# Optimization experiments

Hardware: AMD Instinct MI355X
Metric: run time of the kernel (lower is better)

The kernel has to match this reference:

```python
import jax, jax.numpy as jnp
import numpy as np

SLOPE = 25.0   # fast_sigmoid surrogate slope (affects backward only)
THRESH = 1.0   # snntorch Leaky default threshold

@jax.custom_vjp
def spike(x):
    # Heaviside forward, fast-sigmoid surrogate backward
    return (x > 0).astype(x.dtype)

def _spike_fwd(x):
    return spike(x), x

def _spike_bwd(x, g):
    return (g / (SLOPE * jnp.abs(x) + 1.0) ** 2,)

spike.defvjp(_spike_fwd, _spike_bwd)


def setup_inputs() -> dict:
    key = jax.random.key(0)
    ks = jax.random.split(key, 16)
    B, T, F = 512, 1024, 64
    SNN, H, HOR = 128, 128, 24
    s = 0.05
    inp = {
        "x": jax.random.normal(ks[0], (B, T, F), jnp.float32),
        "proj_w": jax.random.normal(ks[1], (SNN, F), jnp.float32) * s,
        "proj_b": jnp.zeros((SNN,), jnp.float32),
        "beta1": jnp.full((SNN,), 0.9, jnp.float32),
        "beta2": jnp.full((SNN,), 0.9, jnp.float32),
        "gru_w_ih": jax.random.normal(ks[2], (3 * H, F + SNN), jnp.float32) * s,
        "gru_w_hh": jax.random.normal(ks[3], (3 * H, H), jnp.float32) * s,
        "gru_b_ih": jnp.zeros((3 * H,), jnp.float32),
        "gru_b_hh": jnp.zeros((3 * H,), jnp.float32),
        "attn_w1": jax.random.normal(ks[4], (H // 2, H), jnp.float32) * s,
        "attn_b1": jnp.zeros((H // 2,), jnp.float32),
        "attn_w2": jax.random.normal(ks[5], (1, H // 2), jnp.float32) * s,
        "attn_b2": jnp.zeros((1,), jnp.float32),
        "head_w": jax.random.normal(ks[6], (HOR, H), jnp.float32) * s,
        "head_b": jnp.zeros((HOR,), jnp.float32),
    }
    return inp


def reference(x, proj_w, proj_b, beta1, beta2,
              gru_w_ih, gru_w_hh, gru_b_ih, gru_b_hh,
              attn_w1, attn_b1, attn_w2, attn_b2, head_w, head_b):
    b1 = jnp.clip(beta1, 0.0, 0.99)
    b2 = jnp.clip(beta2, 0.0, 0.99)

    delta = x[:, 1:, :] - x[:, :-1, :]   # (B, T-1, F)
    raw = x[:, 1:, :]
    h_s = delta @ proj_w.T + proj_b      # (B, T-1, SNN)

    B = x.shape[0]
    SNN = proj_w.shape[0]

    # snntorch Leaky (subtract reset, reset from previous step's spike):
    # mem_t = beta*mem_{t-1} + in_t - spk_{t-1}*thr ; spk_t = H(mem_t - thr)
    def snn_step(carry, inp_t):
        m1, s1, m2, s2 = carry
        m1 = b1 * m1 + inp_t - s1 * THRESH
        s1n = spike(m1 - THRESH)
        m2 = b2 * m2 + s1n - s2 * THRESH
        s2n = spike(m2 - THRESH)
        return (m1, s1n, m2, s2n), m2

    z = jnp.zeros((B, SNN), x.dtype)
    _, mem_rec = jax.lax.scan(snn_step, (z, z, z, z), jnp.swapaxes(h_s, 0, 1))
    h_snn = jnp.swapaxes(mem_rec, 0, 1)             # (B, T-1, SNN)

    h_comb = jnp.concatenate([raw, h_snn], axis=-1)  # (B, T-1, F+SNN)

    # GRU (PyTorch gate layout: r, z, n)
    H = gru_w_hh.shape[1]
    x_proj = h_comb @ gru_w_ih.T + gru_b_ih          # (B, T-1, 3H)

    def gru_step(h, xp):
        gh = h @ gru_w_hh.T + gru_b_hh
        xr, xz, xn = jnp.split(xp, 3, axis=-1)
        hr, hz, hn = jnp.split(gh, 3, axis=-1)
        r = jax.nn.sigmoid(xr + hr)
        zg = jax.nn.sigmoid(xz + hz)
        n = jnp.tanh(xn + r * hn)
        h_new = (1.0 - zg) * n + zg * h
        return h_new, h_new

    h0 = jnp.zeros((B, H), x.dtype)
    _, gru_seq = jax.lax.scan(gru_step, h0, jnp.swapaxes(x_proj, 0, 1))
    gru_out = jnp.swapaxes(gru_seq, 0, 1)            # (B, T-1, H)

    # Temporal attention over time (dim=1)
    scores = jax.nn.relu(gru_out @ attn_w1.T + attn_b1) @ attn_w2.T + attn_b2  # (B, T-1, 1)
    w = jax.nn.softmax(scores, axis=1)
    h_ann = (w * gru_out).sum(axis=1)                # (B, H)

    return h_ann @ head_w.T + head_b                 # (B, horizon)
```

## Files before the change

kernel.cpp:

```cpp
#include <hip/hip_runtime.h>

typedef unsigned short u16;
typedef __attribute__((ext_vector_type(8))) short short8;
typedef __attribute__((ext_vector_type(4))) float f32x4;

__device__ __forceinline__ u16 f2bf(float f) {
  union { float f; unsigned u; } v; v.f = f;
  unsigned r = v.u + 0x7fffu + ((v.u >> 16) & 1u);
  return (u16)(r >> 16);
}
__device__ __forceinline__ u16 truncbf(float f) {
  union { float f; unsigned u; } v; v.f = f;
  return (u16)(v.u >> 16);
}
__device__ __forceinline__ float bf2f(u16 h) {
  union { unsigned u; float f; } v; v.u = ((unsigned)h) << 16;
  return v.f;
}
__device__ __forceinline__ void gll16(const void* g, void* l) {
  __builtin_amdgcn_global_load_lds((const __attribute__((address_space(1))) unsigned*)g,
                                   (__attribute__((address_space(3))) unsigned*)l, 16, 0, 0);
}
__device__ __forceinline__ void bar_lds() {
  asm volatile("s_waitcnt lgkmcnt(0)" ::: "memory");
  __builtin_amdgcn_s_barrier();
  asm volatile("" ::: "memory");
}

#define BATCH 512
#define TS 1023
#define NF 64
#define NS 128
#define NH 128
#define NG 384
#define NC 192
#define TCH 341

__global__ void k_prep(const float* __restrict__ wih, const float* __restrict__ w1,
                       u16* __restrict__ wihb, u16* __restrict__ w1b) {
  int i = blockIdx.x * 256 + threadIdx.x;
  if (i < NG * NC) wihb[i] = f2bf(wih[i]);
  if (i < 64 * NH) w1b[i] = f2bf(w1[i]);
}

__global__ __launch_bounds__(256, 2) void k_front(const float* __restrict__ x,
                                                  const float* __restrict__ pw,
                                                  const float* __restrict__ pb,
                                                  const float* __restrict__ beta1,
                                                  const float* __restrict__ beta2,
                                                  u16* __restrict__ hcomb) {
  __shared__ float hst[64 * 138];
  const int tid = threadIdx.x, lane = tid & 63, w = tid >> 6;
  const int m16 = lane & 15, quad = lane >> 4;
  const int b = blockIdx.x;
  const float* xb = x + (long)b * 65536;

  const int tm = (w >> 1) * 32, nn = (w & 1) * 64;

  short8 bh[2][4], bl[2][4];
  #pragma unroll
  for (int kc = 0; kc < 2; ++kc)
    #pragma unroll
    for (int ni = 0; ni < 4; ++ni) {
      const float* src = pw + (nn + ni * 16 + m16) * 64 + kc * 32 + quad * 8;
      f32x4 v0 = *(const f32x4*)src;
      f32x4 v1 = *(const f32x4*)(src + 4);
      #pragma unroll
      for (int jj = 0; jj < 8; ++jj) {
        float v = (jj < 4) ? v0[jj & 3] : v1[jj & 3];
        u16 hh = truncbf(v);
        bh[kc][ni][jj] = (short)hh;
        bl[kc][ni][jj] = (short)f2bf(v - bf2f(hh));
      }
    }

  float b1v = 0.f, b2v = 0.f, m1 = 0.f, s1 = 0.f, m2 = 0.f, s2 = 0.f;
  if (tid < 128) {
    b1v = fminf(fmaxf(beta1[tid], 0.f), 0.99f);
    b2v = fminf(fmaxf(beta2[tid], 0.f), 0.99f);
  }
  float pbv[4];
  #pragma unroll
  for (int ni = 0; ni < 4; ++ni) pbv[ni] = pb[nn + ni * 16 + m16];

  for (int tile = 0; tile < 16; ++tile) {
    const int t0 = tile * 64;
    const int tl = (TS - t0 < 64) ? (TS - t0) : 64;

    f32x4 acc[2][4] = {};
    #pragma unroll
    for (int kc = 0; kc < 2; ++kc) {
      short8 ah[2], al[2];
      #pragma unroll
      for (int mi = 0; mi < 2; ++mi) {
        int row = tm + mi * 16 + m16;
        int tA = t0 + row; if (tA > 1022) tA = 1022;
        const float* p0 = xb + (long)tA * 64 + kc * 32 + quad * 8;
        f32x4 lo0 = *(const f32x4*)p0;
        f32x4 lo1 = *(const f32x4*)(p0 + 4);
        f32x4 hi0 = *(const f32x4*)(p0 + 64);
        f32x4 hi1 = *(const f32x4*)(p0 + 68);
        float d[8];
        #pragma unroll
        for (int jj = 0; jj < 4; ++jj) { d[jj] = hi0[jj] - lo0[jj]; d[4 + jj] = hi1[jj] - lo1[jj]; }
        #pragma unroll
        for (int jj = 0; jj < 8; ++jj) {
          u16 hh = truncbf(d[jj]);
          ah[mi][jj] = (short)hh;
          al[mi][jj] = (short)f2bf(d[jj] - bf2f(hh));
        }
      }
      #pragma unroll
      for (int mi = 0; mi < 2; ++mi)
        #pragma unroll
        for (int ni = 0; ni < 4; ++ni) {
          acc[mi][ni] = __builtin_amdgcn_mfma_f32_16x16x32_bf16(ah[mi], bh[kc][ni], acc[mi][ni], 0, 0, 0);
          acc[mi][ni] = __builtin_amdgcn_mfma_f32_16x16x32_bf16(ah[mi], bl[kc][ni], acc[mi][ni], 0, 0, 0);
          acc[mi][ni] = __builtin_amdgcn_mfma_f32_16x16x32_bf16(al[mi], bh[kc][ni], acc[mi][ni], 0, 0, 0);
        }
    }
    #pragma unroll
    for (int mi = 0; mi < 2; ++mi)
      #pragma unroll
      for (int ni = 0; ni < 4; ++ni)
        #pragma unroll
        for (int rr = 0; rr < 4; ++rr)
          hst[(tm + mi * 16 + quad * 4 + rr) * 138 + nn + ni * 16 + m16] = acc[mi][ni][rr] + pbv[ni];
    bar_lds();
    if (tid < 128) {
      const int n = tid;
      u16* dst = hcomb + ((long)t0 * 512 + b) * NC + 64 + n;
      for (int tt = 0; tt < tl; tt += 8) {
        float v[8];
        #pragma unroll
        for (int jj = 0; jj < 8; ++jj) {
          int t = tt + jj; if (t > 63) t = 63;
          v[jj] = hst[t * 138 + n];
        }
        #pragma unroll
        for (int jj = 0; jj < 8; ++jj) {
          int t = tt + jj;
          if (t < tl) {
            m1 = b1v * m1 + v[jj] - s1;
            s1 = (m1 > 1.0f) ? 1.0f : 0.0f;
            m2 = b2v * m2 + s1 - s2;
            s2 = (m2 > 1.0f) ? 1.0f : 0.0f;
            dst[(long)t * (512 * NC)] = f2bf(m2);
          }
        }
      }
    } else {
      const int f = tid & 63, half = (tid >> 6) & 1;
      for (int r = half; r < tl; r += 2)
        hcomb[((long)(t0 + r) * 512 + b) * NC + f] = f2bf(xb[(long)(t0 + r + 1) * 64 + f]);
    }
    bar_lds();
  }
}

__global__ __launch_bounds__(256) void k_xproj(const u16* __restrict__ hc, const u16* __restrict__ wih,
                                               const float* __restrict__ bih, u16* __restrict__ xp) {
  __shared__ alignas(16) u16 As[4096], Bs[4096];
  const int tid = threadIdx.x, lane = tid & 63, w = tid >> 6;
  const int m16 = lane & 15, quad = lane >> 4;
  const long row0 = (long)blockIdx.x * 128;
  const int n0 = blockIdx.y * 128;
  const int wm = (w >> 1) * 64, wn = (w & 1) * 64;
  f32x4 acc[4][4] = {};
  const char* gA = (const char*)hc + (row0 + (lane >> 2)) * (NC * 2) + (lane & 3) * 16;
  const char* gB = (const char*)wih + (long)(n0 + (lane >> 2)) * (NC * 2) + (lane & 3) * 16;
  for (int kc = 0; kc < 6; ++kc) {
    #pragma unroll
    for (int i = 0; i < 2; ++i) {
      int q = i * 4 + w;
      gll16(gA + (long)q * 16 * (NC * 2) + kc * 64, (char*)As + q * 1024);
      gll16(gB + (long)q * 16 * (NC * 2) + kc * 64, (char*)Bs + q * 1024);
    }
    __syncthreads();
    short8 af[4], bfr[4];
    #pragma unroll
    for (int mi = 0; mi < 4; ++mi) af[mi] = *(const short8*)((const char*)As + (wm + mi * 16 + m16) * 64 + quad * 16);
    #pragma unroll
    for (int ni = 0; ni < 4; ++ni) bfr[ni] = *(const short8*)((const char*)Bs + (wn + ni * 16 + m16) * 64 + quad * 16);
    #pragma unroll
    for (int mi = 0; mi < 4; ++mi)
      #pragma unroll
      for (int ni = 0; ni < 4; ++ni)
        acc[mi][ni] = __builtin_amdgcn_mfma_f32_16x16x32_bf16(af[mi], bfr[ni], acc[mi][ni], 0, 0, 0);
    __syncthreads();
  }
  #pragma unroll
  for (int ni = 0; ni < 4; ++ni) {
    int n = n0 + wn + ni * 16 + m16;
    float bias = bih[n];
    #pragma unroll
    for (int mi = 0; mi < 4; ++mi) {
      long r = row0 + wm + mi * 16 + quad * 4;
      #pragma unroll
      for (int rr = 0; rr < 4; ++rr)
        xp[(r + rr) * NG + n] = f2bf(acc[mi][ni][rr] + bias);
    }
  }
}

__global__ __launch_bounds__(256, 1) void k_gru(const u16* __restrict__ xp, const float* __restrict__ whh,
                                                const float* __restrict__ bhh, u16* __restrict__ gout,
                                                float* __restrict__ h_state, int first) {
  __shared__ alignas(16) u16 frag[2 * 2048];
  const int tid = threadIdx.x, lane = tid & 63, w = tid >> 6;
  const int m16 = lane & 15, quad = lane >> 4;
  const long bg0 = (long)blockIdx.x * 2;
  {
    short8 z8 = {};
    *(short8*)((char*)frag + tid * 16) = z8;
    *(short8*)((char*)frag + 4096 + tid * 16) = z8;
  }
  short8 wf[6][4];
  #pragma unroll
  for (int g = 0; g < 3; ++g)
    #pragma unroll
    for (int hh = 0; hh < 2; ++hh)
      #pragma unroll
      for (int c = 0; c < 4; ++c) {
        const float* src = whh + (long)(g * 128 + 32 * w + hh * 16 + m16) * NH + c * 32 + quad * 8;
        short8 v;
        #pragma unroll
        for (int jj = 0; jj < 8; ++jj) v[jj] = (short)f2bf(src[jj]);
        wf[g * 2 + hh][c] = v;
      }
  const int bq = quad & 1, hq = quad >> 1;
  const int j = 32 * w + hq * 16 + m16;
  const long brow = bg0 + bq;
  const float br_ = bhh[j], bz_ = bhh[128 + j], bn_ = bhh[256 + j];
  float h = first ? 0.f : h_state[brow * NH + j];
  const int fragoff = w * 1024 + 64 * bq + 256 * (hq * 2 + (m16 >> 3)) + 2 * (m16 & 7);
  __syncthreads();
  {
    u16 hb0 = f2bf(h);
    *(u16*)((char*)frag + fragoff) = hb0;
    *(u16*)((char*)frag + fragoff + 128) = hb0;
  }
  const u16* xbase = xp + brow * NG + j;
  u16 pr[8], pz[8], pn[8], sbuf[8];
  #pragma unroll
  for (int u = 0; u < 8; ++u) {
    const u16* xr = xbase + (long)u * (512 * NG);
    pr[u] = xr[0]; pz[u] = xr[128]; pn[u] = xr[256];
  }
  __syncthreads();

#define GRU_STEP(T, U)                                                                     \
  {                                                                                        \
    const int cur = ((T) & 1) * 4096, nxt = 4096 - cur;                                    \
    short8 af[4];                                                                          \
    _Pragma("unroll")                                                                      \
    for (int c = 0; c < 4; ++c)                                                            \
      af[c] = *(const short8*)((const char*)frag + cur + c * 1024 + lane * 16);            \
    f32x4 zero = {0.f, 0.f, 0.f, 0.f};                                                     \
    f32x4 accA[6], accB[6];                                                                \
    _Pragma("unroll")                                                                      \
    for (int nt = 0; nt < 6; ++nt) {                                                       \
      accA[nt] = __builtin_amdgcn_mfma_f32_16x16x32_bf16(af[0], wf[nt][0], zero, 0, 0, 0); \
      accB[nt] = __builtin_amdgcn_mfma_f32_16x16x32_bf16(af[2], wf[nt][2], zero, 0, 0, 0); \
    }                                                                                      \
    _Pragma("unroll")                                                                      \
    for (int nt = 0; nt < 4; ++nt) {                                                       \
      accA[nt] = __builtin_amdgcn_mfma_f32_16x16x32_bf16(af[1], wf[nt][1], accA[nt], 0, 0, 0); \
      accB[nt] = __builtin_amdgcn_mfma_f32_16x16x32_bf16(af[3], wf[nt][3], accB[nt], 0, 0, 0); \
    }                                                                                      \
    float ghr = (hq ? (accA[1][0] + accB[1][0]) : (accA[0][0] + accB[0][0])) + br_;        \
    float ghz = (hq ? (accA[3][0] + accB[3][0]) : (accA[2][0] + accB[2][0])) + bz_;        \
    float xrv = bf2f(pr[U]), xzv = bf2f(pz[U]), xnv = bf2f(pn[U]);                         \
    float rg = 1.f / (1.f + __expf(-(xrv + ghr)));                                         \
    float zg = 1.f / (1.f + __expf(-(xzv + ghz)));                                         \
    accA[4] = __builtin_amdgcn_mfma_f32_16x16x32_bf16(af[1], wf[4][1], accA[4], 0, 0, 0);  \
    accB[4] = __builtin_amdgcn_mfma_f32_16x16x32_bf16(af[3], wf[4][3], accB[4], 0, 0, 0);  \
    accA[5] = __builtin_amdgcn_mfma_f32_16x16x32_bf16(af[1], wf[5][1], accA[5], 0, 0, 0);  \
    accB[5] = __builtin_amdgcn_mfma_f32_16x16x32_bf16(af[3], wf[5][3], accB[5], 0, 0, 0);  \
    float ghn = (hq ? (accA[5][0] + accB[5][0]) : (accA[4][0] + accB[4][0])) + bn_;        \
    float niv = xnv + rg * ghn;                                                            \
    float ng = 1.f - 2.f / (1.f + __expf(2.f * niv));                                      \
    h = (1.f - zg) * ng + zg * h;                                                          \
    u16 hb = f2bf(h);                                                                      \
    sbuf[U] = hb;                                                                          \
    *(u16*)((char*)frag + nxt + fragoff) = hb;                                             \
    *(u16*)((char*)frag + nxt + fragoff + 128) = hb;                                       \
    bar_lds();                                                                             \
  }

  for (int t8 = 0; t8 < 336; t8 += 8) {
    if (t8 > 0) {
      #pragma unroll
      for (int u = 0; u < 8; ++u)
        gout[((long)(t8 - 8 + u) * 512 + brow) * NH + j] = sbuf[u];
    }
    u16 npr[8], npz[8], npn[8];
    #pragma unroll
    for (int u = 0; u < 8; ++u) {
      long tp = t8 + 8 + u; if (tp > TCH - 1) tp = TCH - 1;
      const u16* xr = xbase + tp * (512 * NG);
      npr[u] = xr[0]; npz[u] = xr[128]; npn[u] = xr[256];
    }
    GRU_STEP(t8 + 0, 0) GRU_STEP(t8 + 1, 1) GRU_STEP(t8 + 2, 2) GRU_STEP(t8 + 3, 3)
    GRU_STEP(t8 + 4, 4) GRU_STEP(t8 + 5, 5) GRU_STEP(t8 + 6, 6) GRU_STEP(t8 + 7, 7)
    #pragma unroll
    for (int u = 0; u < 8; ++u) { pr[u] = npr[u]; pz[u] = npz[u]; pn[u] = npn[u]; }
  }
  #pragma unroll
  for (int u = 0; u < 8; ++u)
    gout[((long)(328 + u) * 512 + brow) * NH + j] = sbuf[u];
  #pragma unroll
  for (int u = 0; u < 5; ++u) {
    GRU_STEP(336 + u, u)
    gout[((long)(336 + u) * 512 + brow) * NH + j] = sbuf[u];
  }
#undef GRU_STEP
  h_state[brow * NH + j] = h;
}

__global__ __launch_bounds__(256) void k_score(const u16* __restrict__ gbf, const u16* __restrict__ w1,
                                               const float* __restrict__ b1, const float* __restrict__ w2,
                                               const float* __restrict__ b2, float* __restrict__ scores) {
  __shared__ alignas(16) u16 Gs[4096], Ws[2048];
  const int tid = threadIdx.x, lane = tid & 63, w = tid >> 6;
  const int m16 = lane & 15, quad = lane >> 4;
  const long row0 = (long)blockIdx.x * 128;
  f32x4 acc[2][4] = {};
  const char* gG = (const char*)gbf + (row0 + (lane >> 2)) * (NH * 2) + (lane & 3) * 16;
  const char* gW = (const char*)w1 + (long)(w * 16 + (lane >> 2)) * (NH * 2) + (lane & 3) * 16;
  for (int kc = 0; kc < 4; ++kc) {
    #pragma unroll
    for (int i = 0; i < 2; ++i) {
      int q = i * 4 + w;
      gll16(gG + (long)q * 16 * (NH * 2) + kc * 64, (char*)Gs + q * 1024);
    }
    gll16(gW + kc * 64, (char*)Ws + w * 1024);
    __syncthreads();
    short8 af[2], bfr[4];
    #pragma unroll
    for (int mi = 0; mi < 2; ++mi) af[mi] = *(const short8*)((const char*)Gs + (w * 32 + mi * 16 + m16) * 64 + quad * 16);
    #pragma unroll
    for (int ni = 0; ni < 4; ++ni) bfr[ni] = *(const short8*)((const char*)Ws + (ni * 16 + m16) * 64 + quad * 16);
    #pragma unroll
    for (int mi = 0; mi < 2; ++mi)
      #pragma unroll
      for (int ni = 0; ni < 4; ++ni)
        acc[mi][ni] = __builtin_amdgcn_mfma_f32_16x16x32_bf16(af[mi], bfr[ni], acc[mi][ni], 0, 0, 0);
    __syncthreads();
  }
  float b2v = b2[0];
  float w2v[4], b1v[4];
  #pragma unroll
  for (int ni = 0; ni < 4; ++ni) { w2v[ni] = w2[ni * 16 + m16]; b1v[ni] = b1[ni * 16 + m16]; }
  #pragma unroll
  for (int mi = 0; mi < 2; ++mi) {
    #pragma unroll
    for (int rr = 0; rr < 4; ++rr) {
      float v = 0.f;
      #pragma unroll
      for (int ni = 0; ni < 4; ++ni) {
        float hv = acc[mi][ni][rr] + b1v[ni];
        hv = hv > 0.f ? hv : 0.f;
        v = fmaf(hv, w2v[ni], v);
      }
      v += __shfl_xor(v, 1, 64); v += __shfl_xor(v, 2, 64);
      v += __shfl_xor(v, 4, 64); v += __shfl_xor(v, 8, 64);
      if (m16 == 0) scores[row0 + w * 32 + mi * 16 + quad * 4 + rr] = v + b2v;
    }
  }
}

__global__ __launch_bounds__(256) void k_attn(const float* __restrict__ scores, const u16* __restrict__ gout,
                                              const float* __restrict__ headw, const float* __restrict__ headb,
                                              float* __restrict__ out) {
  __shared__ float sc[TS];
  __shared__ float red[8];
  __shared__ float part[8][132];
  __shared__ float hann[128];
  const int tid = threadIdx.x, lane = tid & 63, w = tid >> 6;
  const long b = blockIdx.x;
  const float* srow = scores + b;
  float s0[4];
  #pragma unroll
  for (int i = 0; i < 4; ++i) {
    int t = tid + i * 256;
    s0[i] = (t < TS) ? srow[(long)t * 512] : -1e30f;
  }
  float mx = fmaxf(fmaxf(s0[0], s0[1]), fmaxf(s0[2], s0[3]));
  #pragma unroll
  for (int off = 32; off > 0; off >>= 1) mx = fmaxf(mx, __shfl_xor(mx, off, 64));
  if (lane == 0) red[w] = mx;
  __syncthreads();
  mx = fmaxf(fmaxf(red[0], red[1]), fmaxf(red[2], red[3]));
  float sum = 0.f;
  #pragma unroll
  for (int i = 0; i < 4; ++i) {
    int t = tid + i * 256;
    if (t < TS) { float e = __expf(s0[i] - mx); sc[t] = e; sum += e; }
  }
  #pragma unroll
  for (int off = 32; off > 0; off >>= 1) sum += __shfl_xor(sum, off, 64);
  if (lane == 0) red[4 + w] = sum;
  __syncthreads();
  float inv = 1.f / (red[4] + red[5] + red[6] + red[7]);
  const int jg = tid & 31, sl = tid >> 5;
  float acc[4] = {0.f, 0.f, 0.f, 0.f};
  const u16* gbase = gout + b * NH + jg * 4;
  for (int t = sl; t < TS; t += 8) {
    float wt = sc[t];
    ushort4 g4 = *(const ushort4*)(gbase + (long)t * (512 * NH));
    acc[0] = fmaf(wt, bf2f(g4.x), acc[0]);
    acc[1] = fmaf(wt, bf2f(g4.y), acc[1]);
    acc[2] = fmaf(wt, bf2f(g4.z), acc[2]);
    acc[3] = fmaf(wt, bf2f(g4.w), acc[3]);
  }
  #pragma unroll
  for (int i = 0; i < 4; ++i) part[sl][jg * 4 + i] = acc[i];
  __syncthreads();
  if (tid < 128) {
    float v = 0.f;
    #pragma unroll
    for (int s = 0; s < 8; ++s) v += part[s][tid];
    hann[tid] = v * inv;
  }
  __syncthreads();
  if (tid < 24) {
    float a = headb[tid];
    const float* hwr = headw + tid * 128;
    for (int k = 0; k < 128; k += 4) {
      float4 h4 = *(const float4*)&hann[k];
      float4 w4 = *(const float4*)&hwr[k];
      a = fmaf(h4.x, w4.x, a); a = fmaf(h4.y, w4.y, a);
      a = fmaf(h4.z, w4.z, a); a = fmaf(h4.w, w4.w, a);
    }
    out[b * 24 + tid] = a;
  }
}

extern "C" void kernel_launch(void* const* d_in, const int* in_sizes, int n_in,
                              void* d_out, int out_size, void* d_ws, size_t ws_size,
                              hipStream_t stream) {
  const float* x      = (const float*)d_in[0];
  const float* proj_w = (const float*)d_in[1];
  const float* proj_b = (const float*)d_in[2];
  const float* beta1  = (const float*)d_in[3];
  const float* beta2  = (const float*)d_in[4];
  const float* gwih   = (const float*)d_in[5];
  const float* gwhh   = (const float*)d_in[6];
  const float* gbih   = (const float*)d_in[7];
  const float* gbhh   = (const float*)d_in[8];
  const float* aw1    = (const float*)d_in[9];
  const float* ab1    = (const float*)d_in[10];
  const float* aw2    = (const float*)d_in[11];
  const float* ab2    = (const float*)d_in[12];
  const float* hw     = (const float*)d_in[13];
  const float* hb     = (const float*)d_in[14];
  float* out = (float*)d_out;
  char* ws = (char*)d_ws;

  u16*   hcomb  = (u16*)(ws);
  u16*   xpbuf  = (u16*)(ws + 201129984L);
  u16*   gru    = (u16*)(ws + 335216640L);
  float* scores = (float*)(ws + 469303296L);
  u16*   wihb   = (u16*)(ws + 471398400L);
  u16*   w1b    = (u16*)(ws + 471545856L);
  float* hstate = (float*)(ws + 471562240L);

  k_prep<<<288, 256, 0, stream>>>(gwih, aw1, wihb, w1b);
  k_front<<<512, 256, 0, stream>>>(x, proj_w, proj_b, beta1, beta2, hcomb);
  for (int c = 0; c < 3; ++c) {
    long rowbase = (long)c * TCH * 512;
    k_xproj<<<dim3(1364, 3), 256, 0, stream>>>(hcomb + rowbase * NC, wihb, gbih, xpbuf);
    k_gru<<<256, 256, 0, stream>>>(xpbuf, gwhh, gbhh, gru + rowbase * NH, hstate, c == 0 ? 1 : 0);
  }
  k_score<<<4092, 256, 0, stream>>>(gru, w1b, ab1, aw2, ab2, scores);
  k_attn<<<512, 256, 0, stream>>>(scores, gru, hw, hb, out);
}
```

Measured before the change: 1.048 ms.

## Overlap attention score computation of previous chunk with GRU recurrence blocks

The GRU launch for chunks 1 and 2 now carries extra blocks that compute attention scores for the previous chunk's GRU output. This lets the low-occupancy sequential GRU run alongside otherwise idle CUs, and only the last chunk's scores go to a standalone k_score launch. The GRU step also issues all six gate MFMA chains up front instead of interleaving the n-gate ones after the sigmoids. Its LDS-only barrier becomes a full __syncthreads. The extra shared memory for the score tiles, and score blocks competing for CUs, may slow the latency-critical GRU blocks.

```diff
diff --git a/kernel.cpp b/kernel.cpp
--- a/kernel.cpp
+++ b/kernel.cpp
@@ -203,10 +203,78 @@
   }
 }
 
+__device__ __forceinline__ void score_body(long row0, const u16* __restrict__ gbf, const u16* __restrict__ w1,
+                                           const float* __restrict__ b1, const float* __restrict__ w2,
+                                           const float* __restrict__ b2, float* __restrict__ scores,
+                                           u16* Gs, u16* Ws) {
+  const int tid = threadIdx.x, lane = tid & 63, w = tid >> 6;
+  const int m16 = lane & 15, quad = lane >> 4;
+  f32x4 acc[2][4] = {};
+  const char* gG = (const char*)gbf + (row0 + (lane >> 2)) * (NH * 2) + (lane & 3) * 16;
+  const char* gW = (const char*)w1 + (long)(w * 16 + (lane >> 2)) * (NH * 2) + (lane & 3) * 16;
+  for (int kc = 0; kc < 4; ++kc) {
+    #pragma unroll
+    for (int i = 0; i < 2; ++i) {
+      int q = i * 4 + w;
+      gll16(gG + (long)q * 16 * (NH * 2) + kc * 64, (char*)Gs + q * 1024);
+    }
+    gll16(gW + kc * 64, (char*)Ws + w * 1024);
+    __syncthreads();
+    short8 af[2], bfr[4];
+    #pragma unroll
+    for (int mi = 0; mi < 2; ++mi) af[mi] = *(const short8*)((const char*)Gs + (w * 32 + mi * 16 + m16) * 64 + quad * 16);
+    #pragma unroll
+    for (int ni = 0; ni < 4; ++ni) bfr[ni] = *(const short8*)((const char*)Ws + (ni * 16 + m16) * 64 + quad * 16);
+    #pragma unroll
+    for (int mi = 0; mi < 2; ++mi)
+      #pragma unroll
+      for (int ni = 0; ni < 4; ++ni)
+        acc[mi][ni] = __builtin_amdgcn_mfma_f32_16x16x32_bf16(af[mi], bfr[ni], acc[mi][ni], 0, 0, 0);
+    __syncthreads();
+  }
+  float b2v = b2[0];
+  float w2v[4], b1v[4];
+  #pragma unroll
+  for (int ni = 0; ni < 4; ++ni) { w2v[ni] = w2[ni * 16 + m16]; b1v[ni] = b1[ni * 16 + m16]; }
+  #pragma unroll
+  for (int mi = 0; mi < 2; ++mi) {
+    #pragma unroll
+    for (int rr = 0; rr < 4; ++rr) {
+      float v = 0.f;
+      #pragma unroll
+      for (int ni = 0; ni < 4; ++ni) {
+        float hv = acc[mi][ni][rr] + b1v[ni];
+        hv = hv > 0.f ? hv : 0.f;
+        v = fmaf(hv, w2v[ni], v);
+      }
+      v += __shfl_xor(v, 1, 64); v += __shfl_xor(v, 2, 64);
+      v += __shfl_xor(v, 4, 64); v += __shfl_xor(v, 8, 64);
+      if (m16 == 0) scores[row0 + w * 32 + mi * 16 + quad * 4 + rr] = v + b2v;
+    }
+  }
+}
+
+__global__ __launch_bounds__(256) void k_score(const u16* __restrict__ gbf, const u16* __restrict__ w1,
+                                               const float* __restrict__ b1, const float* __restrict__ w2,
+                                               const float* __restrict__ b2, float* __restrict__ scores,
+                                               long row_base) {
+  __shared__ alignas(16) u16 Gs[4096], Ws[2048];
+  score_body(row_base + (long)blockIdx.x * 128, gbf, w1, b1, w2, b2, scores, Gs, Ws);
+}
+
 __global__ __launch_bounds__(256, 1) void k_gru(const u16* __restrict__ xp, const float* __restrict__ whh,
                                                 const float* __restrict__ bhh, u16* __restrict__ gout,
-                                                float* __restrict__ h_state, int first) {
+                                                float* __restrict__ h_state, int first,
+                                                const u16* __restrict__ gbf, const u16* __restrict__ w1,
+                                                const float* __restrict__ b1, const float* __restrict__ w2,
+                                                const float* __restrict__ b2, float* __restrict__ scores,
+                                                long score_base) {
   __shared__ alignas(16) u16 frag[2 * 2048];
+  __shared__ alignas(16) u16 Gs[4096], Ws[2048];
+  if (blockIdx.x >= 256) {
+    score_body(score_base + (long)(blockIdx.x - 256) * 128, gbf, w1, b1, w2, b2, scores, Gs, Ws);
+    return;
+  }
   const int tid = threadIdx.x, lane = tid & 63, w = tid >> 6;
   const int m16 = lane & 15, quad = lane >> 4;
   const long bg0 = (long)blockIdx.x * 2;
@@ -264,20 +332,16 @@
       accB[nt] = __builtin_amdgcn_mfma_f32_16x16x32_bf16(af[2], wf[nt][2], zero, 0, 0, 0); \
     }                                                                                      \
     _Pragma("unroll")                                                                      \
-    for (int nt = 0; nt < 4; ++nt) {                                                       \
+    for (int nt = 0; nt < 6; ++nt) {                                                       \
       accA[nt] = __builtin_amdgcn_mfma_f32_16x16x32_bf16(af[1], wf[nt][1], accA[nt], 0, 0, 0); \
       accB[nt] = __builtin_amdgcn_mfma_f32_16x16x32_bf16(af[3], wf[nt][3], accB[nt], 0, 0, 0); \
     }                                                                                      \
     float ghr = (hq ? (accA[1][0] + accB[1][0]) : (accA[0][0] + accB[0][0])) + br_;        \
     float ghz = (hq ? (accA[3][0] + accB[3][0]) : (accA[2][0] + accB[2][0])) + bz_;        \
+    float ghn = (hq ? (accA[5][0] + accB[5][0]) : (accA[4][0] + accB[4][0])) + bn_;        \
     float xrv = bf2f(pr[U]), xzv = bf2f(pz[U]), xnv = bf2f(pn[U]);                         \
     float rg = 1.f / (1.f + __expf(-(xrv + ghr)));                                         \
     float zg = 1.f / (1.f + __expf(-(xzv + ghz)));                                         \
-    accA[4] = __builtin_amdgcn_mfma_f32_16x16x32_bf16(af[1], wf[4][1], accA[4], 0, 0, 0);  \
-    accB[4] = __builtin_amdgcn_mfma_f32_16x16x32_bf16(af[3], wf[4][3], accB[4], 0, 0, 0);  \
-    accA[5] = __builtin_amdgcn_mfma_f32_16x16x32_bf16(af[1], wf[5][1], accA[5], 0, 0, 0);  \
-    accB[5] = __builtin_amdgcn_mfma_f32_16x16x32_bf16(af[3], wf[5][3], accB[5], 0, 0, 0);  \
-    float ghn = (hq ? (accA[5][0] + accB[5][0]) : (accA[4][0] + accB[4][0])) + bn_;        \
     float niv = xnv + rg * ghn;                                                            \
     float ng = 1.f - 2.f / (1.f + __expf(2.f * niv));                                      \
     h = (1.f - zg) * ng + zg * h;                                                          \
@@ -285,7 +349,7 @@
     sbuf[U] = hb;                                                                          \
     *(u16*)((char*)frag + nxt + fragoff) = hb;                                             \
     *(u16*)((char*)frag + nxt + fragoff + 128) = hb;                                       \
-    bar_lds();                                                                             \
+    __syncthreads();                                                                       \
   }
 
   for (int t8 = 0; t8 < 336; t8 += 8) {
@@ -316,58 +380,6 @@
   }
 #undef GRU_STEP
   h_state[brow * NH + j] = h;
-}
-
-__global__ __launch_bounds__(256) void k_score(const u16* __restrict__ gbf, const u16* __restrict__ w1,
-                                               const float* __restrict__ b1, const float* __restrict__ w2,
-                                               const float* __restrict__ b2, float* __restrict__ scores) {
-  __shared__ alignas(16) u16 Gs[4096], Ws[2048];
-  const int tid = threadIdx.x, lane = tid & 63, w = tid >> 6;
-  const int m16 = lane & 15, quad = lane >> 4;
-  const long row0 = (long)blockIdx.x * 128;
-  f32x4 acc[2][4] = {};
-  const char* gG = (const char*)gbf + (row0 + (lane >> 2)) * (NH * 2) + (lane & 3) * 16;
-  const char* gW = (const char*)w1 + (long)(w * 16 + (lane >> 2)) * (NH * 2) + (lane & 3) * 16;
-  for (int kc = 0; kc < 4; ++kc) {
-    #pragma unroll
-    for (int i = 0; i < 2; ++i) {
-      int q = i * 4 + w;
-      gll16(gG + (long)q * 16 * (NH * 2) + kc * 64, (char*)Gs + q * 1024);
-    }
-    gll16(gW + kc * 64, (char*)Ws + w * 1024);
-    __syncthreads();
-    short8 af[2], bfr[4];
-    #pragma unroll
-    for (int mi = 0; mi < 2; ++mi) af[mi] = *(const short8*)((const char*)Gs + (w * 32 + mi * 16 + m16) * 64 + quad * 16);
-    #pragma unroll
-    for (int ni = 0; ni < 4; ++ni) bfr[ni] = *(const short8*)((const char*)Ws + (ni * 16 + m16) * 64 + quad * 16);
-    #pragma unroll
-    for (int mi = 0; mi < 2; ++mi)
-      #pragma unroll
-      for (int ni = 0; ni < 4; ++ni)
-        acc[mi][ni] = __builtin_amdgcn_mfma_f32_16x16x32_bf16(af[mi], bfr[ni], acc[mi][ni], 0, 0, 0);
-    __syncthreads();
-  }
-  float b2v = b2[0];
-  float w2v[4], b1v[4];
-  #pragma unroll
-  for (int ni = 0; ni < 4; ++ni) { w2v[ni] = w2[ni * 16 + m16]; b1v[ni] = b1[ni * 16 + m16]; }
-  #pragma unroll
-  for (int mi = 0; mi < 2; ++mi) {
-    #pragma unroll
-    for (int rr = 0; rr < 4; ++rr) {
-      float v = 0.f;
-      #pragma unroll
-      for (int ni = 0; ni < 4; ++ni) {
-        float hv = acc[mi][ni][rr] + b1v[ni];
-        hv = hv > 0.f ? hv : 0.f;
-        v = fmaf(hv, w2v[ni], v);
-      }
-      v += __shfl_xor(v, 1, 64); v += __shfl_xor(v, 2, 64);
-      v += __shfl_xor(v, 4, 64); v += __shfl_xor(v, 8, 64);
-      if (m16 == 0) scores[row0 + w * 32 + mi * 16 + quad * 4 + rr] = v + b2v;
-    }
-  }
 }
 
 __global__ __launch_bounds__(256) void k_attn(const float* __restrict__ scores, const u16* __restrict__ gout,
@@ -471,8 +483,11 @@
   for (int c = 0; c < 3; ++c) {
     long rowbase = (long)c * TCH * 512;
     k_xproj<<<dim3(1364, 3), 256, 0, stream>>>(hcomb + rowbase * NC, wihb, gbih, xpbuf);
-    k_gru<<<256, 256, 0, stream>>>(xpbuf, gwhh, gbhh, gru + rowbase * NH, hstate, c == 0 ? 1 : 0);
-  }
-  k_score<<<4092, 256, 0, stream>>>(gru, w1b, ab1, aw2, ab2, scores);
+    int grid = (c == 0) ? 256 : 256 + 1364;
+    long score_base = (long)(c - 1) * TCH * 512;
+    k_gru<<<grid, 256, 0, stream>>>(xpbuf, gwhh, gbhh, gru + rowbase * NH, hstate, c == 0 ? 1 : 0,
+                                    gru, w1b, ab1, aw2, ab2, scores, score_base);
+  }
+  k_score<<<1364, 256, 0, stream>>>(gru, w1b, ab1, aw2, ab2, scores, 2L * TCH * 512);
   k_attn<<<512, 256, 0, stream>>>(scores, gru, hw, hb, out);
 }
```

Result: slower. 1.101 ms (+5.1%).
